# Performance work log

Measured on AMD Instinct MI355X. Metric: run time of the kernel, lower is better.

## Reference

```python
import jax, jax.numpy as jnp
import numpy as np

B, N, C, K = 8, 4096, 512, 150

def setup_inputs() -> dict:
    key = jax.random.key(0)
    ks = jax.random.split(key, 10)
    std_c = float(np.sqrt(2.0 / C))
    x = jax.random.normal(ks[0], (B, N, C), dtype=jnp.float32)
    Wq = jax.random.normal(ks[1], (K, C), dtype=jnp.float32) * std_c
    bq = jnp.zeros((K,), dtype=jnp.float32)
    Wk = jax.random.normal(ks[2], (K, C), dtype=jnp.float32) * std_c
    bk = jnp.zeros((K,), dtype=jnp.float32)
    Wv = jax.random.normal(ks[3], (C, C), dtype=jnp.float32) * std_c
    bv = jnp.zeros((C,), dtype=jnp.float32)
    # original inits mlp_res to zeros; use small random so output is nontrivial
    Wres = jax.random.normal(ks[4], (C, C), dtype=jnp.float32) * (0.02)
    bres = jnp.zeros((C,), dtype=jnp.float32)
    gamma = jnp.full((1,), 0.5, dtype=jnp.float32)  # original init is 0; nonzero for testing
    return {"x": x, "Wq": Wq, "bq": bq, "Wk": Wk, "bk": bk,
            "Wv": Wv, "bv": bv, "Wres": Wres, "bres": bres, "gamma": gamma}

def reference(x, Wq, bq, Wk, bk, Wv, bv, Wres, bres, gamma):
    # seg_map: (B,N,K); seg_ft: (B,N,K); feats: (B,N,C)
    seg_map = jnp.einsum('bnc,kc->bnk', x, Wq) + bq
    seg_ft = jnp.einsum('bnc,kc->bnk', x, Wk) + bk
    v = jnp.einsum('bnc,dc->bnd', x, Wv) + bv
    # low-rank QK^T -> (B,N,N), unscaled, row softmax
    score = jnp.einsum('bnk,bmk->bnm', seg_map, seg_ft)
    score = jax.nn.softmax(score, axis=-1)
    feats = jnp.einsum('bnm,bmd->bnd', score, v)
    feats = jnp.einsum('bnd,ed->bne', feats, Wres) + bres
    # dropout omitted (inference); gamma-gated residual
    feat_map = gamma * feats + x
    return (seg_map, feat_map)
```

## Files before the change

kernel.cpp:

```cpp
#include <hip/hip_runtime.h>
#include <cstdint>
#include <cstddef>

#define M_ROWS 32768
#define CDIM   512
#define KRANK  150
#define KPAD   160

typedef __bf16 bf16x8 __attribute__((ext_vector_type(8)));
typedef float  f32x4  __attribute__((ext_vector_type(4)));

union U16B { uint4 u; bf16x8 b; };
static __device__ __forceinline__ bf16x8 u2b(uint4 u) { U16B x; x.u = u; return x.b; }

static __device__ __forceinline__ unsigned short f2bf(float f) {
  uint32_t u = __float_as_uint(f);
  u += 0x7fffu + ((u >> 16) & 1u);
  return (unsigned short)(u >> 16);
}

static __device__ __forceinline__ void cvt8(float4 a, float4 b, uint4& h, uint4& l) {
  float v[8] = {a.x, a.y, a.z, a.w, b.x, b.y, b.z, b.w};
  unsigned short hs[8], ls[8];
#pragma unroll
  for (int i = 0; i < 8; ++i) {
    hs[i] = f2bf(v[i]);
    const float hf = __uint_as_float((uint32_t)hs[i] << 16);
    ls[i] = f2bf(v[i] - hf);
  }
  h = *(uint4*)&hs[0];
  l = *(uint4*)&ls[0];
}

template<int MODE>
__global__ __launch_bounds__(512, 4)
void mgemm_nt(const float* __restrict__ A, const float* __restrict__ W,
              const float* __restrict__ bias, float* __restrict__ out,
              const float* __restrict__ xres, const float* __restrict__ gammap,
              unsigned short* __restrict__ aux)
{
  __shared__ __align__(16) unsigned short lds[24576];
  const int tid = threadIdx.x;
  const int m0  = blockIdx.y * 128;
  const int n0b = blockIdx.x * 256;

  const int srow = tid >> 2, sk4 = tid & 3;
  const int sa16 = ((srow >> 1) << 3) + ((((srow & 1) << 2) | sk4) ^ ((srow >> 1) & 7));
  const float* ap  = A + (size_t)(m0 + srow) * 512 + sk4 * 8;
  const float* bp0 = W + (size_t)(n0b + srow) * 512 + sk4 * 8;
  const float* bp1 = W + (size_t)(n0b + 128 + srow) * 512 + sk4 * 8;
  const bool b1ok = (MODE == 1 || MODE == 4) || (srow < (KRANK - 128));

  const int lane = tid & 63, w = tid >> 6;
  const int wm = w >> 2, wn = w & 3;
  const int cq = lane & 15, quad = lane >> 4;
  const int fsub = (((cq & 1) << 2) | quad) ^ (cq >> 1);
  const int a16 = wm * 256 + ((cq >> 1) << 3) + fsub;
  const int b16 = wn * 256 + ((cq >> 1) << 3) + fsub;

  f32x4 acc[4][4];
#pragma unroll
  for (int i = 0; i < 4; ++i)
#pragma unroll
    for (int j = 0; j < 4; ++j) acc[i][j] = (f32x4){0.f, 0.f, 0.f, 0.f};

  for (int kt = 0; kt < 512; kt += 32) {
    const float4 av0 = *(const float4*)(ap + kt);
    const float4 av1 = *(const float4*)(ap + kt + 4);
    const float4 bv0 = *(const float4*)(bp0 + kt);
    const float4 bv1 = *(const float4*)(bp0 + kt + 4);
    float4 cv0 = make_float4(0.f, 0.f, 0.f, 0.f), cv1 = cv0;
    if (b1ok) { cv0 = *(const float4*)(bp1 + kt); cv1 = *(const float4*)(bp1 + kt + 4); }
    uint4 ahi, alo, bhi, blo, chi, clo;
    cvt8(av0, av1, ahi, alo);
    cvt8(bv0, bv1, bhi, blo);
    cvt8(cv0, cv1, chi, clo);

    __syncthreads();
    *(uint4*)&lds[        sa16 * 8]        = ahi;
    *(uint4*)&lds[4096  + sa16 * 8]        = alo;
    *(uint4*)&lds[8192  + sa16 * 8]        = bhi;
    *(uint4*)&lds[16384 + sa16 * 8]        = blo;
    *(uint4*)&lds[8192  + sa16 * 8 + 4096] = chi;
    *(uint4*)&lds[16384 + sa16 * 8 + 4096] = clo;
    __syncthreads();

    bf16x8 ah[4], al_[4];
#pragma unroll
    for (int i = 0; i < 4; ++i) {
      ah[i]  = u2b(*(const uint4*)&lds[       (a16 + i * 64) * 8]);
      al_[i] = u2b(*(const uint4*)&lds[4096 + (a16 + i * 64) * 8]);
    }
#pragma unroll
    for (int j = 0; j < 4; ++j) {
      const bf16x8 bh = u2b(*(const uint4*)&lds[8192  + (b16 + j * 64) * 8]);
      const bf16x8 bl = u2b(*(const uint4*)&lds[16384 + (b16 + j * 64) * 8]);
#pragma unroll
      for (int i = 0; i < 4; ++i) {
        acc[i][j] = __builtin_amdgcn_mfma_f32_16x16x32_bf16(ah[i],  bh, acc[i][j], 0, 0, 0);
        acc[i][j] = __builtin_amdgcn_mfma_f32_16x16x32_bf16(al_[i], bh, acc[i][j], 0, 0, 0);
        acc[i][j] = __builtin_amdgcn_mfma_f32_16x16x32_bf16(ah[i],  bl, acc[i][j], 0, 0, 0);
      }
    }
  }

  const int mb = m0 + wm * 64 + quad * 4;
  const int nb = n0b + wn * 64 + cq;

  if (MODE == 1) {
    const float g = gammap[0];
#pragma unroll
    for (int j = 0; j < 4; ++j) {
      const float bvj = bias[nb + j * 16];
#pragma unroll
      for (int i = 0; i < 4; ++i) {
#pragma unroll
        for (int r = 0; r < 4; ++r) {
          const size_t off = (size_t)(mb + i * 16 + r) * 512 + (nb + j * 16);
          out[off] = fmaf(g, acc[i][j][r] + bvj, xres[off]);
        }
      }
    }
  } else if (MODE == 4) {
    const int b = m0 >> 12;
    const int key0 = (m0 & 4095) + wm * 64 + quad * 4;
#pragma unroll
    for (int j = 0; j < 4; ++j) {
      const float bvj = bias[nb + j * 16];
      const size_t rowo = (size_t)(b * 512 + nb + j * 16) * 4096;
#pragma unroll
      for (int i = 0; i < 4; ++i) {
        unsigned short o4[4];
#pragma unroll
        for (int r = 0; r < 4; ++r) o4[r] = f2bf(acc[i][j][r] + bvj);
        uint2 o;
        o.x = (unsigned int)o4[0] | ((unsigned int)o4[1] << 16);
        o.y = (unsigned int)o4[2] | ((unsigned int)o4[3] << 16);
        *(uint2*)&aux[rowo + key0 + i * 16] = o;
      }
    }
  } else {
#pragma unroll
    for (int j = 0; j < 4; ++j) {
      const int n = nb + j * 16;
      if (n < KPAD) {
        const float bvj = (n < KRANK) ? bias[n] : 0.f;
#pragma unroll
        for (int i = 0; i < 4; ++i) {
#pragma unroll
          for (int r = 0; r < 4; ++r) {
            const int m = mb + i * 16 + r;
            float v = (n < KRANK) ? (acc[i][j][r] + bvj) : 0.f;
            if (MODE == 2 && n < KRANK) out[(size_t)m * KRANK + n] = v;
            const unsigned short h = f2bf(v);
            aux[(size_t)m * 320 + n] = h;
            const float hf = __uint_as_float(((uint32_t)h) << 16);
            aux[(size_t)m * 320 + 160 + n] = f2bf(v - hf);
          }
        }
      }
    }
  }
}

__global__ __launch_bounds__(512, 2)
void attn_mfma(const unsigned short* __restrict__ Qc,
               const unsigned short* __restrict__ Kc,
               const unsigned short* __restrict__ VT,
               float* __restrict__ O)
{
  __shared__ __align__(16) unsigned short smem[32064];
  unsigned short* klds = smem;
  unsigned short* vtl  = smem + 10496;
  unsigned short* plds = smem + 26944;

  const int bid = blockIdx.x;
  const int b   = bid & 7;
  const int qt  = bid >> 3;
  const int r0  = (b << 12) + qt * 128;

  const int tid  = threadIdx.x;
  const int w    = tid >> 6;
  const int lane = tid & 63;
  const int quad = lane >> 4;
  const int cq   = lane & 15;

  bf16x8 qhi[5], qlo[5];
  {
    const size_t qrow = (size_t)(r0 + w * 16 + cq) * 320;
#pragma unroll
    for (int c = 0; c < 5; ++c) {
      qhi[c] = u2b(*(const uint4*)(Qc + qrow + c * 32 + quad * 8));
      qlo[c] = u2b(*(const uint4*)(Qc + qrow + 160 + c * 32 + quad * 8));
    }
  }

  f32x4 acc4[32];
#pragma unroll
  for (int i = 0; i < 32; ++i) acc4[i] = (f32x4){0.f, 0.f, 0.f, 0.f};
  float mreg[4], lreg[4];
#pragma unroll
  for (int r = 0; r < 4; ++r) { mreg[r] = -3.0e38f; lreg[r] = 0.f; }

  const int vqd = (tid & 3) * 8;
  const int vc  = tid >> 2;
  const int vwb = (tid & 3) * 4112 + vc * 8;
  const int vrb = quad * 4112 + cq * 8;

  const int krow0 = tid / 40,          kc0 = (tid - krow0 * 40) * 8;
  const int krow1 = (tid + 512) / 40,  kc1 = ((tid + 512) - krow1 * 40) * 8;
  const int krow2 = (tid + 1024) / 40, kc2 = ((tid + 1024) - krow2 * 40) * 8;

  uint4 pk0, pk1, pk2, pv0, pv1, pv2, pv3;
  const unsigned short* kbase = Kc + (size_t)(b * 4096) * 320;
  const unsigned short* vbase = VT + ((size_t)(b * 512 + vc)) * 4096 + vqd;
  {
    pk0 = *(const uint4*)(kbase + (size_t)tid * 8);
    pk1 = *(const uint4*)(kbase + (size_t)(tid + 512) * 8);
    if (tid < 256) pk2 = *(const uint4*)(kbase + (size_t)(tid + 1024) * 8);
    pv0 = *(const uint4*)(vbase);
    pv1 = *(const uint4*)(vbase + (size_t)128 * 4096);
    pv2 = *(const uint4*)(vbase + (size_t)256 * 4096);
    pv3 = *(const uint4*)(vbase + (size_t)384 * 4096);
  }

  for (int kt = 0; kt < 128; ++kt) {
    __syncthreads();

    *(uint4*)&klds[krow0 * 328 + kc0] = pk0;
    *(uint4*)&klds[krow1 * 328 + kc1] = pk1;
    if (tid < 256) *(uint4*)&klds[krow2 * 328 + kc2] = pk2;
    *(uint4*)&vtl[vwb]        = pv0;
    *(uint4*)&vtl[vwb + 1024] = pv1;
    *(uint4*)&vtl[vwb + 2048] = pv2;
    *(uint4*)&vtl[vwb + 3072] = pv3;

    __syncthreads();

    {
      const int ktn = (kt < 127) ? kt + 1 : 127;
      pk0 = *(const uint4*)(kbase + (size_t)(ktn * 32 * 320) + (size_t)tid * 8);
      pk1 = *(const uint4*)(kbase + (size_t)(ktn * 32 * 320) + (size_t)(tid + 512) * 8);
      if (tid < 256) pk2 = *(const uint4*)(kbase + (size_t)(ktn * 32 * 320) + (size_t)(tid + 1024) * 8);
      pv0 = *(const uint4*)(vbase + ktn * 32);
      pv1 = *(const uint4*)(vbase + (size_t)128 * 4096 + ktn * 32);
      pv2 = *(const uint4*)(vbase + (size_t)256 * 4096 + ktn * 32);
      pv3 = *(const uint4*)(vbase + (size_t)384 * 4096 + ktn * 32);
    }

    f32x4 S0 = (f32x4){0.f, 0.f, 0.f, 0.f};
    f32x4 S1 = (f32x4){0.f, 0.f, 0.f, 0.f};
#pragma unroll
    for (int c = 0; c < 5; ++c) {
      const int ko = c * 32 + quad * 8;
      const bf16x8 kh0 = u2b(*(const uint4*)&klds[cq * 328 + ko]);
      const bf16x8 kl0 = u2b(*(const uint4*)&klds[cq * 328 + 160 + ko]);
      const bf16x8 kh1 = u2b(*(const uint4*)&klds[(16 + cq) * 328 + ko]);
      const bf16x8 kl1 = u2b(*(const uint4*)&klds[(16 + cq) * 328 + 160 + ko]);
      S0 = __builtin_amdgcn_mfma_f32_16x16x32_bf16(qhi[c], kh0, S0, 0, 0, 0);
      S1 = __builtin_amdgcn_mfma_f32_16x16x32_bf16(qhi[c], kh1, S1, 0, 0, 0);
      S0 = __builtin_amdgcn_mfma_f32_16x16x32_bf16(qhi[c], kl0, S0, 0, 0, 0);
      S1 = __builtin_amdgcn_mfma_f32_16x16x32_bf16(qhi[c], kl1, S1, 0, 0, 0);
      S0 = __builtin_amdgcn_mfma_f32_16x16x32_bf16(qlo[c], kh0, S0, 0, 0, 0);
      S1 = __builtin_amdgcn_mfma_f32_16x16x32_bf16(qlo[c], kh1, S1, 0, 0, 0);
    }

    unsigned short* pw = plds + w * 640;
    float alph[4];
    bool upd = false;
#pragma unroll
    for (int r = 0; r < 4; ++r) {
      const float s0 = S0[r], s1 = S1[r];
      float t = fmaxf(s0, s1);
      t = fmaxf(t, __shfl_xor(t, 1));
      t = fmaxf(t, __shfl_xor(t, 2));
      t = fmaxf(t, __shfl_xor(t, 4));
      t = fmaxf(t, __shfl_xor(t, 8));
      const float mo = mreg[r];
      const float mn = fmaxf(mo, t);
      upd = upd || (mn > mo);
      const float al = __expf(mo - mn);
      const float p0 = __expf(s0 - mn);
      const float p1 = __expf(s1 - mn);
      float ts = p0 + p1;
      ts += __shfl_xor(ts, 1);
      ts += __shfl_xor(ts, 2);
      ts += __shfl_xor(ts, 4);
      ts += __shfl_xor(ts, 8);
      lreg[r] = lreg[r] * al + ts;
      mreg[r] = mn;
      alph[r] = al;
      const int prow = (quad * 4 + r) * 40;
      pw[prow + cq]      = f2bf(p0);
      pw[prow + 16 + cq] = f2bf(p1);
    }

    if (__any(upd)) {
#pragma unroll
      for (int i = 0; i < 32; ++i) {
        acc4[i][0] *= alph[0]; acc4[i][1] *= alph[1];
        acc4[i][2] *= alph[2]; acc4[i][3] *= alph[3];
      }
    }

    const bf16x8 pa = u2b(*(const uint4*)&pw[cq * 40 + quad * 8]);
#pragma unroll
    for (int i = 0; i < 32; ++i) {
      const bf16x8 vb = u2b(*(const uint4*)&vtl[vrb + i * 128]);
      acc4[i] = __builtin_amdgcn_mfma_f32_16x16x32_bf16(pa, vb, acc4[i], 0, 0, 0);
    }
  }

  float inv[4];
#pragma unroll
  for (int r = 0; r < 4; ++r) inv[r] = 1.f / lreg[r];

  __syncthreads();
  float* ep = (float*)smem + w * 1088;
  const int r0w = r0 + w * 16;
#pragma unroll
  for (int qtr = 0; qtr < 8; ++qtr) {
#pragma unroll
    for (int ii = 0; ii < 4; ++ii)
#pragma unroll
      for (int r = 0; r < 4; ++r)
        ep[(quad * 4 + r) * 68 + ii * 16 + cq] = acc4[qtr * 4 + ii][r] * inv[r];
#pragma unroll
    for (int t = 0; t < 4; ++t) {
      const int flat4 = t * 64 + lane;
      const int row = flat4 >> 4;
      const int c4 = flat4 & 15;
      const float4 val = *(const float4*)&ep[row * 68 + c4 * 4];
      *(float4*)&O[(size_t)(r0w + row) * CDIM + qtr * 64 + c4 * 4] = val;
    }
  }
}

extern "C" void kernel_launch(void* const* d_in, const int* in_sizes, int n_in,
                              void* d_out, int out_size, void* d_ws, size_t ws_size,
                              hipStream_t stream)
{
  const float* x     = (const float*)d_in[0];
  const float* Wq    = (const float*)d_in[1];
  const float* bq    = (const float*)d_in[2];
  const float* Wk    = (const float*)d_in[3];
  const float* bk    = (const float*)d_in[4];
  const float* Wv    = (const float*)d_in[5];
  const float* bv    = (const float*)d_in[6];
  const float* Wres  = (const float*)d_in[7];
  const float* bres  = (const float*)d_in[8];
  const float* gamma = (const float*)d_in[9];

  float* seg_map  = (float*)d_out;
  float* feat_map = seg_map + (size_t)M_ROWS * KRANK;

  unsigned short* Qcomb = (unsigned short*)d_ws;
  unsigned short* Kcomb = Qcomb + (size_t)M_ROWS * 320;
  unsigned short* VTb   = Kcomb + (size_t)M_ROWS * 320;
  float*          feats = (float*)(VTb + (size_t)M_ROWS * CDIM);

  mgemm_nt<2><<<dim3(1, 256), dim3(512), 0, stream>>>(x, Wq, bq, seg_map, nullptr, nullptr, Qcomb);
  mgemm_nt<3><<<dim3(1, 256), dim3(512), 0, stream>>>(x, Wk, bk, nullptr, nullptr, nullptr, Kcomb);
  mgemm_nt<4><<<dim3(2, 256), dim3(512), 0, stream>>>(x, Wv, bv, nullptr, nullptr, nullptr, VTb);
  attn_mfma<<<dim3(256), dim3(512), 0, stream>>>(Qcomb, Kcomb, VTb, feats);
  mgemm_nt<1><<<dim3(2, 256), dim3(512), 0, stream>>>(feats, Wres, bres, feat_map, x, gamma, nullptr);
}
```

Baseline: 811.2 us.

## Pre-convert weights to swizzled bf16 images, async-load to LDS, lazy softmax rescale

A new kernel converts Wq/Wk/Wv/Wres once per call into pre-swizzled hi/lo bf16 tile images. The projection GEMMs then copy those images straight into LDS with global_load_lds instead of loading fp32 weights and splitting them in every block. This removes the repeated weight conversion and the extra register traffic. In attention, MFMA sections get raised wave priority, and the running max is only updated when the new max exceeds the old one by more than 8. That skips most accumulator rescales and exps, at the cost of a looser bound on the exponent range.

```diff
diff --git a/kernel.cpp b/kernel.cpp
--- a/kernel.cpp
+++ b/kernel.cpp
@@ -32,9 +32,53 @@
   l = *(uint4*)&ls[0];
 }
 
+static __device__ __forceinline__ void glds16(const void* g, void* l) {
+  __builtin_amdgcn_global_load_lds(
+      (const __attribute__((address_space(1))) unsigned int*)g,
+      (__attribute__((address_space(3))) unsigned int*)l, 16, 0, 0);
+}
+
+static __device__ __forceinline__ int sa16f(int row, int k4) {
+  return ((row >> 1) << 3) + ((((row & 1) << 2) | k4) ^ ((row >> 1) & 7));
+}
+
+__global__ __launch_bounds__(512)
+void cvt_w(const float* __restrict__ Wv, const float* __restrict__ Wres,
+           const float* __restrict__ Wq, const float* __restrict__ Wk,
+           unsigned short* __restrict__ WvC, unsigned short* __restrict__ WresC,
+           unsigned short* __restrict__ WqC, unsigned short* __restrict__ WkC)
+{
+  int job = blockIdx.x;
+  const float* W; unsigned short* img; int N;
+  if (job < 32)      { W = Wv;   img = WvC;   N = 512; }
+  else if (job < 64) { W = Wres; img = WresC; N = 512; job -= 32; }
+  else if (job < 80) { W = Wq;   img = WqC;   N = KRANK; job -= 64; }
+  else               { W = Wk;   img = WkC;   N = KRANK; job -= 80; }
+  const int nt = (N == 512) ? (job >> 4) : 0;
+  const int kt = job & 15;
+
+  const int tid = threadIdx.x;
+  const int srow = tid >> 2, sk4 = tid & 3;
+  const int sa = sa16f(srow, sk4);
+  unsigned short* ib = img + (size_t)(nt * 16 + kt) * 16384;
+#pragma unroll
+  for (int h = 0; h < 2; ++h) {
+    const int row = nt * 256 + h * 128 + srow;
+    float4 v0 = make_float4(0.f, 0.f, 0.f, 0.f), v1 = v0;
+    if (row < N) {
+      v0 = *(const float4*)&W[(size_t)row * 512 + kt * 32 + sk4 * 8];
+      v1 = *(const float4*)&W[(size_t)row * 512 + kt * 32 + sk4 * 8 + 4];
+    }
+    uint4 h4, l4; cvt8(v0, v1, h4, l4);
+    const int cell = h * 512 + sa;
+    *(uint4*)&ib[(size_t)cell * 8]          = h4;
+    *(uint4*)&ib[(size_t)(1024 + cell) * 8] = l4;
+  }
+}
+
 template<int MODE>
 __global__ __launch_bounds__(512, 4)
-void mgemm_nt(const float* __restrict__ A, const float* __restrict__ W,
+void mgemm_nt(const float* __restrict__ A, const unsigned short* __restrict__ Wimg,
               const float* __restrict__ bias, float* __restrict__ out,
               const float* __restrict__ xres, const float* __restrict__ gammap,
               unsigned short* __restrict__ aux)
@@ -42,14 +86,10 @@
   __shared__ __align__(16) unsigned short lds[24576];
   const int tid = threadIdx.x;
   const int m0  = blockIdx.y * 128;
-  const int n0b = blockIdx.x * 256;
 
   const int srow = tid >> 2, sk4 = tid & 3;
-  const int sa16 = ((srow >> 1) << 3) + ((((srow & 1) << 2) | sk4) ^ ((srow >> 1) & 7));
-  const float* ap  = A + (size_t)(m0 + srow) * 512 + sk4 * 8;
-  const float* bp0 = W + (size_t)(n0b + srow) * 512 + sk4 * 8;
-  const float* bp1 = W + (size_t)(n0b + 128 + srow) * 512 + sk4 * 8;
-  const bool b1ok = (MODE == 1 || MODE == 4) || (srow < (KRANK - 128));
+  const int sa16 = sa16f(srow, sk4);
+  const float* ap = A + (size_t)(m0 + srow) * 512 + sk4 * 8;
 
   const int lane = tid & 63, w = tid >> 6;
   const int wm = w >> 2, wn = w & 3;
@@ -58,6 +98,9 @@
   const int a16 = wm * 256 + ((cq >> 1) << 3) + fsub;
   const int b16 = wn * 256 + ((cq >> 1) << 3) + fsub;
 
+  const unsigned short* ibase = Wimg + (size_t)(blockIdx.x * 16) * 16384
+                              + (size_t)(w * 64 + lane) * 8;
+
   f32x4 acc[4][4];
 #pragma unroll
   for (int i = 0; i < 4; ++i)
@@ -67,22 +110,16 @@
   for (int kt = 0; kt < 512; kt += 32) {
     const float4 av0 = *(const float4*)(ap + kt);
     const float4 av1 = *(const float4*)(ap + kt + 4);
-    const float4 bv0 = *(const float4*)(bp0 + kt);
-    const float4 bv1 = *(const float4*)(bp0 + kt + 4);
-    float4 cv0 = make_float4(0.f, 0.f, 0.f, 0.f), cv1 = cv0;
-    if (b1ok) { cv0 = *(const float4*)(bp1 + kt); cv1 = *(const float4*)(bp1 + kt + 4); }
-    uint4 ahi, alo, bhi, blo, chi, clo;
+    uint4 ahi, alo;
     cvt8(av0, av1, ahi, alo);
-    cvt8(bv0, bv1, bhi, blo);
-    cvt8(cv0, cv1, chi, clo);
 
     __syncthreads();
-    *(uint4*)&lds[        sa16 * 8]        = ahi;
-    *(uint4*)&lds[4096  + sa16 * 8]        = alo;
-    *(uint4*)&lds[8192  + sa16 * 8]        = bhi;
-    *(uint4*)&lds[16384 + sa16 * 8]        = blo;
-    *(uint4*)&lds[8192  + sa16 * 8 + 4096] = chi;
-    *(uint4*)&lds[16384 + sa16 * 8 + 4096] = clo;
+    *(uint4*)&lds[       sa16 * 8] = ahi;
+    *(uint4*)&lds[4096 + sa16 * 8] = alo;
+    const unsigned short* src = ibase + (size_t)(kt >> 5) * 16384;
+#pragma unroll
+    for (int c = 0; c < 4; ++c)
+      glds16(src + (size_t)c * 4096, &lds[8192 + (c * 512 + w * 64) * 8]);
     __syncthreads();
 
     bf16x8 ah[4], al_[4];
@@ -104,6 +141,7 @@
     }
   }
 
+  const int n0b = blockIdx.x * 256;
   const int mb = m0 + wm * 64 + quad * 4;
   const int nb = n0b + wn * 64 + cq;
 
@@ -250,6 +288,7 @@
 
     f32x4 S0 = (f32x4){0.f, 0.f, 0.f, 0.f};
     f32x4 S1 = (f32x4){0.f, 0.f, 0.f, 0.f};
+    __builtin_amdgcn_s_setprio(1);
 #pragma unroll
     for (int c = 0; c < 5; ++c) {
       const int ko = c * 32 + quad * 8;
@@ -264,6 +303,7 @@
       S0 = __builtin_amdgcn_mfma_f32_16x16x32_bf16(qlo[c], kh0, S0, 0, 0, 0);
       S1 = __builtin_amdgcn_mfma_f32_16x16x32_bf16(qlo[c], kh1, S1, 0, 0, 0);
     }
+    __builtin_amdgcn_s_setprio(0);
 
     unsigned short* pw = plds + w * 640;
     float alph[4];
@@ -277,9 +317,10 @@
       t = fmaxf(t, __shfl_xor(t, 4));
       t = fmaxf(t, __shfl_xor(t, 8));
       const float mo = mreg[r];
-      const float mn = fmaxf(mo, t);
-      upd = upd || (mn > mo);
-      const float al = __expf(mo - mn);
+      const bool need = (t > mo + 8.f);
+      const float mn = need ? t : mo;
+      upd = upd || need;
+      const float al = need ? __expf(mo - mn) : 1.f;
       const float p0 = __expf(s0 - mn);
       const float p1 = __expf(s1 - mn);
       float ts = p0 + p1;
@@ -304,11 +345,13 @@
     }
 
     const bf16x8 pa = u2b(*(const uint4*)&pw[cq * 40 + quad * 8]);
+    __builtin_amdgcn_s_setprio(1);
 #pragma unroll
     for (int i = 0; i < 32; ++i) {
       const bf16x8 vb = u2b(*(const uint4*)&vtl[vrb + i * 128]);
       acc4[i] = __builtin_amdgcn_mfma_f32_16x16x32_bf16(pa, vb, acc4[i], 0, 0, 0);
     }
+    __builtin_amdgcn_s_setprio(0);
   }
 
   float inv[4];
@@ -358,10 +401,15 @@
   unsigned short* Kcomb = Qcomb + (size_t)M_ROWS * 320;
   unsigned short* VTb   = Kcomb + (size_t)M_ROWS * 320;
   float*          feats = (float*)(VTb + (size_t)M_ROWS * CDIM);
-
-  mgemm_nt<2><<<dim3(1, 256), dim3(512), 0, stream>>>(x, Wq, bq, seg_map, nullptr, nullptr, Qcomb);
-  mgemm_nt<3><<<dim3(1, 256), dim3(512), 0, stream>>>(x, Wk, bk, nullptr, nullptr, nullptr, Kcomb);
-  mgemm_nt<4><<<dim3(2, 256), dim3(512), 0, stream>>>(x, Wv, bv, nullptr, nullptr, nullptr, VTb);
+  unsigned short* WvC   = (unsigned short*)(feats + (size_t)M_ROWS * CDIM);
+  unsigned short* WresC = WvC   + (size_t)2 * 16 * 16384;
+  unsigned short* WqC   = WresC + (size_t)2 * 16 * 16384;
+  unsigned short* WkC   = WqC   + (size_t)16 * 16384;
+
+  cvt_w<<<dim3(96), dim3(512), 0, stream>>>(Wv, Wres, Wq, Wk, WvC, WresC, WqC, WkC);
+  mgemm_nt<2><<<dim3(1, 256), dim3(512), 0, stream>>>(x, WqC, bq, seg_map, nullptr, nullptr, Qcomb);
+  mgemm_nt<3><<<dim3(1, 256), dim3(512), 0, stream>>>(x, WkC, bk, nullptr, nullptr, nullptr, Kcomb);
+  mgemm_nt<4><<<dim3(2, 256), dim3(512), 0, stream>>>(x, WvC, bv, nullptr, nullptr, nullptr, VTb);
   attn_mfma<<<dim3(256), dim3(512), 0, stream>>>(Qcomb, Kcomb, VTb, feats);
-  mgemm_nt<1><<<dim3(2, 256), dim3(512), 0, stream>>>(feats, Wres, bres, feat_map, x, gamma, nullptr);
-}
+  mgemm_nt<1><<<dim3(2, 256), dim3(512), 0, stream>>>(feats, WresC, bres, feat_map, x, gamma, nullptr);
+}
```

Result: faster. 771.6 us (-4.9%).
